# Kernel optimization log

Hardware: AMD Instinct MI355X
Metric: run time of the kernel (lower is better)

The kernel has to match this reference:

```python
import jax, jax.numpy as jnp
import numpy as np

KSIZE = 11
EPS = 1e-6

def _gauss_kernel(k=KSIZE, sigma=None):
    if sigma is None:
        sigma = k
    p = k // 2
    coords = np.arange(k) - p
    yy, xx = np.meshgrid(coords, coords, indexing='ij')
    g = np.exp(-(xx ** 2 + yy ** 2) / (2.0 * sigma ** 2))
    g = g / g.sum()
    return jnp.asarray(g, dtype=jnp.float32)

def setup_inputs() -> dict:
    key = jax.random.key(0)
    k1, k2 = jax.random.split(key)
    B, C, H, W = 16, 64, 256, 256
    x = jax.random.normal(k1, (B, C, H, W), dtype=jnp.float32)
    y = jax.random.normal(k2, (B, C, H, W), dtype=jnp.float32)
    gauss = _gauss_kernel()
    return {"x": x, "y": y, "gauss": gauss}

def reference(x, y, gauss):
    # Fused form: weighted local sums of x^2, y^2, x*y are SAME-padded
    # cross-correlations of the channel-summed products with the Gaussian.
    # This matches torch Unfold(padding=K//2) zero-padding semantics exactly.
    B, C, H, W = x.shape
    # channel-reduced local statistics inputs: [3, B, H, W]
    s = jnp.stack([
        jnp.sum(x * x, axis=1),
        jnp.sum(x * y, axis=1),
        jnp.sum(y * y, axis=1),
    ], axis=0)
    inp = s.reshape(3 * B, 1, H, W)              # NCHW
    ker = gauss[None, None, :, :]                # OIHW (symmetric -> corr==conv)
    out = jax.lax.conv_general_dilated(
        inp, ker, window_strides=(1, 1), padding='SAME',
        dimension_numbers=('NCHW', 'OIHW', 'NCHW'))
    xx, xy, yy = out.reshape(3, B, H, W)
    x_norm = jnp.sqrt(xx)
    y_norm = jnp.sqrt(yy)
    return xy / (x_norm * y_norm + EPS)
```

## Files before the change

kernel.cpp:

```cpp
#include <hip/hip_runtime.h>
#include <math.h>

constexpr int B = 16, C = 64, H = 256, W = 256;
constexpr int HW = H * W;
constexpr int BHW = B * HW;
constexpr int K = 11, P = 5;
#define EPS 1e-6f

__global__ __launch_bounds__(256) void k_reduce(
    const float* __restrict__ x, const float* __restrict__ y,
    float* __restrict__ s )
{
    const int GPI = HW / 4;
    __shared__ float4 lds[3][128];

    int t = threadIdx.x;
    int half = t >> 7;
    int lane = t & 127;
    int gidx = blockIdx.x * 128 + lane;
    int b = gidx >> 14;
    int g = gidx & (GPI - 1);

    const float4* x4 = (const float4*)x + ((size_t)b * C + half * 32) * GPI + g;
    const float4* y4 = (const float4*)y + ((size_t)b * C + half * 32) * GPI + g;

    float4 axx = make_float4(0.f, 0.f, 0.f, 0.f);
    float4 axy = axx, ayy = axx;

#pragma unroll 8
    for (int c = 0; c < 32; ++c) {
        float4 xv = x4[c * GPI];
        float4 yv = y4[c * GPI];
        axx.x += xv.x * xv.x; axx.y += xv.y * xv.y;
        axx.z += xv.z * xv.z; axx.w += xv.w * xv.w;
        axy.x += xv.x * yv.x; axy.y += xv.y * yv.y;
        axy.z += xv.z * yv.z; axy.w += xv.w * yv.w;
        ayy.x += yv.x * yv.x; ayy.y += yv.y * yv.y;
        ayy.z += yv.z * yv.z; ayy.w += yv.w * yv.w;
    }

    if (half) {
        lds[0][lane] = axx;
        lds[1][lane] = axy;
        lds[2][lane] = ayy;
    }
    __syncthreads();
    if (!half) {
        float4 bxx = lds[0][lane], bxy = lds[1][lane], byy = lds[2][lane];
        axx.x += bxx.x; axx.y += bxx.y; axx.z += bxx.z; axx.w += bxx.w;
        axy.x += bxy.x; axy.y += bxy.y; axy.z += bxy.z; axy.w += bxy.w;
        ayy.x += byy.x; ayy.y += byy.y; ayy.z += byy.z; ayy.w += byy.w;

        float4* s4 = (float4*)s;
        s4[gidx]                  = axx;
        s4[(BHW / 4) + gidx]      = axy;
        s4[2 * (BHW / 4) + gidx]  = ayy;
    }
}

constexpr int TH = 32, TW = 32;
constexpr int RH = TH + K - 1;
constexpr int RW = TW + K - 1;
constexpr int RWP = RW + 2;

__global__ __launch_bounds__(256) void k_blur_combine(
    const float* __restrict__ s, const float* __restrict__ gauss,
    float* __restrict__ out )
{
    __shared__ float raw[3][RH][RWP];
    __shared__ float hb[3][RH][TW];

    int t = threadIdx.x;
    int blk = blockIdx.x;
    int b  = blk >> 6;
    int th = (blk >> 3) & 7;
    int tw = blk & 7;
    int h0 = th * TH, w0 = tw * TW;

    float inv = 1.0f / sqrtf(gauss[5 * K + 5]);
    float wr[K], wc[K];
#pragma unroll
    for (int j = 0; j < K; ++j) wr[j] = gauss[5 * K + j] * inv;
#pragma unroll
    for (int i = 0; i < K; ++i) wc[i] = gauss[i * K + 5] * inv;

    for (int m = 0; m < 3; ++m) {
        const float* sp = s + m * BHW + b * HW;
        for (int i = t; i < RH * RW; i += 256) {
            int r = i / RW;
            int c2 = i - r * RW;
            int h = h0 - P + r;
            int w = w0 - P + c2;
            float v = 0.f;
            if (h >= 0 && h < H && w >= 0 && w < W) v = sp[h * W + w];
            raw[m][r][c2] = v;
        }
    }
    __syncthreads();

    for (int i = t; i < 3 * RH * TW; i += 256) {
        int m = i / (RH * TW);
        int rem = i - m * (RH * TW);
        int r = rem >> 5;
        int cc = rem & (TW - 1);
        float a = 0.f;
#pragma unroll
        for (int j = 0; j < K; ++j) a += wr[j] * raw[m][r][cc + j];
        hb[m][r][cc] = a;
    }
    __syncthreads();

#pragma unroll
    for (int k = 0; k < 4; ++k) {
        int idx = t + k * 256;
        int rr = idx >> 5;
        int cc = idx & (TW - 1);
        float axx = 0.f, axy = 0.f, ayy = 0.f;
#pragma unroll
        for (int i = 0; i < K; ++i) {
            float wi = wc[i];
            axx += wi * hb[0][rr + i][cc];
            axy += wi * hb[1][rr + i][cc];
            ayy += wi * hb[2][rr + i][cc];
        }
        out[b * HW + (h0 + rr) * W + (w0 + cc)] = axy / (sqrtf(axx) * sqrtf(ayy) + EPS);
    }
}

extern "C" void kernel_launch(void* const* d_in, const int* in_sizes, int n_in,
                              void* d_out, int out_size, void* d_ws, size_t ws_size,
                              hipStream_t stream) {
    const float* x     = (const float*)d_in[0];
    const float* y     = (const float*)d_in[1];
    const float* gauss = (const float*)d_in[2];
    float* out = (float*)d_out;

    float* s = (float*)d_ws;

    k_reduce<<<(B * (HW / 4)) / 128, 256, 0, stream>>>(x, y, s);
    k_blur_combine<<<B * (H / TH) * (W / TW), 256, 0, stream>>>(s, gauss, out);
}
```

Measured before the change: 528.7 us.

## Prefetch-pipeline channel reduction with nontemporal loads and widen blur tiles

The reduction kernel now has each thread sum all 64 channels on its own, which removes the split-half LDS exchange and the barrier. It keeps an 8-deep register ring of nontemporal vector loads so more memory requests are in flight and the streamed inputs do not pollute the cache. The blur kernel tile widens from 32x32 to 32x64, which cuts the halo overhead per output. The costs are halved grid parallelism in the reduction, higher register pressure, and larger LDS use per blur block, which may lower occupancy.

```diff
diff --git a/kernel.cpp b/kernel.cpp
--- a/kernel.cpp
+++ b/kernel.cpp
@@ -7,58 +7,49 @@
 constexpr int K = 11, P = 5;
 #define EPS 1e-6f
 
+typedef float v4 __attribute__((ext_vector_type(4)));
+
 __global__ __launch_bounds__(256) void k_reduce(
     const float* __restrict__ x, const float* __restrict__ y,
     float* __restrict__ s )
 {
     const int GPI = HW / 4;
-    __shared__ float4 lds[3][128];
+    int idx = blockIdx.x * 256 + threadIdx.x;
+    int b = idx >> 14;
+    int g = idx & (GPI - 1);
 
-    int t = threadIdx.x;
-    int half = t >> 7;
-    int lane = t & 127;
-    int gidx = blockIdx.x * 128 + lane;
-    int b = gidx >> 14;
-    int g = gidx & (GPI - 1);
+    const v4* x4 = (const v4*)x + (size_t)b * C * GPI + g;
+    const v4* y4 = (const v4*)y + (size_t)b * C * GPI + g;
 
-    const float4* x4 = (const float4*)x + ((size_t)b * C + half * 32) * GPI + g;
-    const float4* y4 = (const float4*)y + ((size_t)b * C + half * 32) * GPI + g;
+    v4 axx = {0.f, 0.f, 0.f, 0.f};
+    v4 axy = axx, ayy = axx;
 
-    float4 axx = make_float4(0.f, 0.f, 0.f, 0.f);
-    float4 axy = axx, ayy = axx;
-
-#pragma unroll 8
-    for (int c = 0; c < 32; ++c) {
-        float4 xv = x4[c * GPI];
-        float4 yv = y4[c * GPI];
-        axx.x += xv.x * xv.x; axx.y += xv.y * xv.y;
-        axx.z += xv.z * xv.z; axx.w += xv.w * xv.w;
-        axy.x += xv.x * yv.x; axy.y += xv.y * yv.y;
-        axy.z += xv.z * yv.z; axy.w += xv.w * yv.w;
-        ayy.x += yv.x * yv.x; ayy.y += yv.y * yv.y;
-        ayy.z += yv.z * yv.z; ayy.w += yv.w * yv.w;
+    v4 bx[8], by[8];
+#pragma unroll
+    for (int i = 0; i < 8; ++i) {
+        bx[i] = __builtin_nontemporal_load(x4 + i * GPI);
+        by[i] = __builtin_nontemporal_load(y4 + i * GPI);
+    }
+#pragma unroll
+    for (int c = 0; c < C; ++c) {
+        v4 xv = bx[c & 7];
+        v4 yv = by[c & 7];
+        if (c + 8 < C) {
+            bx[c & 7] = __builtin_nontemporal_load(x4 + (c + 8) * GPI);
+            by[c & 7] = __builtin_nontemporal_load(y4 + (c + 8) * GPI);
+        }
+        axx += xv * xv;
+        axy += xv * yv;
+        ayy += yv * yv;
     }
 
-    if (half) {
-        lds[0][lane] = axx;
-        lds[1][lane] = axy;
-        lds[2][lane] = ayy;
-    }
-    __syncthreads();
-    if (!half) {
-        float4 bxx = lds[0][lane], bxy = lds[1][lane], byy = lds[2][lane];
-        axx.x += bxx.x; axx.y += bxx.y; axx.z += bxx.z; axx.w += bxx.w;
-        axy.x += bxy.x; axy.y += bxy.y; axy.z += bxy.z; axy.w += bxy.w;
-        ayy.x += byy.x; ayy.y += byy.y; ayy.z += byy.z; ayy.w += byy.w;
-
-        float4* s4 = (float4*)s;
-        s4[gidx]                  = axx;
-        s4[(BHW / 4) + gidx]      = axy;
-        s4[2 * (BHW / 4) + gidx]  = ayy;
-    }
+    v4* s4 = (v4*)s;
+    s4[idx]                 = axx;
+    s4[(BHW / 4) + idx]     = axy;
+    s4[2 * (BHW / 4) + idx] = ayy;
 }
 
-constexpr int TH = 32, TW = 32;
+constexpr int TH = 32, TW = 64;
 constexpr int RH = TH + K - 1;
 constexpr int RW = TW + K - 1;
 constexpr int RWP = RW + 2;
@@ -72,9 +63,9 @@
 
     int t = threadIdx.x;
     int blk = blockIdx.x;
-    int b  = blk >> 6;
-    int th = (blk >> 3) & 7;
-    int tw = blk & 7;
+    int b  = blk >> 5;
+    int th = (blk >> 2) & 7;
+    int tw = blk & 3;
     int h0 = th * TH, w0 = tw * TW;
 
     float inv = 1.0f / sqrtf(gauss[5 * K + 5]);
@@ -87,7 +78,7 @@
     for (int m = 0; m < 3; ++m) {
         const float* sp = s + m * BHW + b * HW;
         for (int i = t; i < RH * RW; i += 256) {
-            int r = i / RW;
+            int r  = i / RW;
             int c2 = i - r * RW;
             int h = h0 - P + r;
             int w = w0 - P + c2;
@@ -99,9 +90,9 @@
     __syncthreads();
 
     for (int i = t; i < 3 * RH * TW; i += 256) {
-        int m = i / (RH * TW);
+        int m   = i / (RH * TW);
         int rem = i - m * (RH * TW);
-        int r = rem >> 5;
+        int r  = rem >> 6;
         int cc = rem & (TW - 1);
         float a = 0.f;
 #pragma unroll
@@ -111,9 +102,9 @@
     __syncthreads();
 
 #pragma unroll
-    for (int k = 0; k < 4; ++k) {
+    for (int k = 0; k < 8; ++k) {
         int idx = t + k * 256;
-        int rr = idx >> 5;
+        int rr = idx >> 6;
         int cc = idx & (TW - 1);
         float axx = 0.f, axy = 0.f, ayy = 0.f;
 #pragma unroll
@@ -137,6 +128,6 @@
 
     float* s = (float*)d_ws;
 
-    k_reduce<<<(B * (HW / 4)) / 128, 256, 0, stream>>>(x, y, s);
+    k_reduce<<<B * (HW / 4) / 256, 256, 0, stream>>>(x, y, s);
     k_blur_combine<<<B * (H / TH) * (W / TW), 256, 0, stream>>>(s, gauss, out);
 }
```

After: 513.3 us. 1.03x faster.
